# Kernel optimization log

Hardware: AMD Instinct MI355X
Metric: run time of the kernel (lower is better)

Reference implementation:

```python
import jax, jax.numpy as jnp
import numpy as np

N_NODES = 100000
N_EDGES = 3200000
D = 128
N_SUPPORTS = 2
N_LAYERS = 2


def setup_inputs() -> dict:
    key = jax.random.key(0)
    ks = jax.random.split(key, 6)
    x = jax.random.normal(ks[0], (1, N_NODES, D), dtype=jnp.float32)
    # small init scale to keep tanh out of saturation
    Ws = jax.random.normal(ks[1], (N_SUPPORTS, N_LAYERS, D, D), dtype=jnp.float32) * 0.05
    bs = jax.random.normal(ks[2], (N_SUPPORTS, N_LAYERS, D), dtype=jnp.float32) * 0.01
    vals = jax.random.uniform(ks[3], (N_SUPPORTS, N_EDGES), dtype=jnp.float32) / 32.0
    rows = jax.random.randint(ks[4], (N_SUPPORTS, N_EDGES), 0, N_NODES, dtype=jnp.int32)
    cols = jax.random.randint(ks[5], (N_SUPPORTS, N_EDGES), 0, N_NODES, dtype=jnp.int32)
    return {"x": x, "Ws": Ws, "bs": bs, "vals": vals, "rows": rows, "cols": cols}


def _spmm(vals, rows, cols, h, n):
    # y[r] += v * h[c]  (sparse COO matrix times dense feature matrix)
    return jax.ops.segment_sum(vals[:, None] * h[cols], rows, num_segments=n)


def reference(x, Ws, bs, vals, rows, cols):
    # AbstractGCN (siml GCN) with residual=True, nodes=[128,128,128],
    # activations=['tanh','tanh'] -> per-layer acts become [tanh, identity],
    # final tanh applied after residual sum; shortcut = identity (in==out dims).
    xb = x[0]  # batch size 1; supports are per-sample
    h_sum = jnp.zeros_like(xb)
    for s in range(N_SUPPORTS):
        h = xb
        for l in range(N_LAYERS):
            h = h @ Ws[s, l].T + bs[s, l]          # torch.nn.Linear
            h = _spmm(vals[s], rows[s], cols[s], h, N_NODES)
            if l == 0:
                h = jnp.tanh(h)                     # identity on last layer
        h_sum = h_sum + h
    out = jnp.tanh(h_sum + xb)                      # residual + final activation
    return out[None]  # stack over batch -> [1, N, D]
```

## Files before the change

kernel.cpp:

```cpp
#include <hip/hip_runtime.h>

#define NN 100000
#define DD 128
#define NE 3200000
#define SCAN_B 1024

__global__ __launch_bounds__(256) void gemm_xwt(const float* __restrict__ h,
                                                const float* __restrict__ W,
                                                const float* __restrict__ b,
                                                float* __restrict__ g) {
    __shared__ float Wl[128 * 128];
    const int t = threadIdx.x;
    for (int i = t * 4; i < 128 * 128; i += 256 * 4) {
        const int n = i >> 7;
        const int k = i & 127;
        const float4 w = *(const float4*)&W[i];
        *(float4*)&Wl[(n << 7) + ((((k >> 2) ^ (n & 7)) << 2))] = w;
    }
    __syncthreads();

    const int tc = t & 15;
    const int tr = t >> 4;
    const int r0 = blockIdx.x * 64 + tr * 4;

    int rr[4];
#pragma unroll
    for (int j = 0; j < 4; ++j) rr[j] = min(r0 + j, NN - 1);

    float acc[4][8];
#pragma unroll
    for (int i = 0; i < 8; ++i) {
        const float bv = b[tc + 16 * i];
#pragma unroll
        for (int j = 0; j < 4; ++j) acc[j][i] = bv;
    }

#pragma unroll 2
    for (int k0 = 0; k0 < 128; k0 += 4) {
        float4 hv[4];
#pragma unroll
        for (int j = 0; j < 4; ++j)
            hv[j] = *(const float4*)&h[(size_t)rr[j] * DD + k0];
#pragma unroll
        for (int i = 0; i < 8; ++i) {
            const int n = tc + 16 * i;
            const float4 wv =
                *(const float4*)&Wl[(n << 7) + ((((k0 >> 2) ^ (n & 7)) << 2))];
#pragma unroll
            for (int j = 0; j < 4; ++j) {
                acc[j][i] += hv[j].x * wv.x;
                acc[j][i] += hv[j].y * wv.y;
                acc[j][i] += hv[j].z * wv.z;
                acc[j][i] += hv[j].w * wv.w;
            }
        }
    }

#pragma unroll
    for (int j = 0; j < 4; ++j) {
        const int r = r0 + j;
        if (r < NN) {
#pragma unroll
            for (int i = 0; i < 8; ++i)
                g[(size_t)r * DD + tc + 16 * i] = acc[j][i];
        }
    }
}

__global__ __launch_bounds__(256) void edge_count2(const int* __restrict__ rows,
                                                   int* __restrict__ cnt2) {
    for (int e = blockIdx.x * 256 + threadIdx.x; e < 2 * NE;
         e += gridDim.x * 256) {
        const int soff = (e >= NE) ? NN : 0;
        atomicAdd(&cnt2[soff + rows[e]], 1);
    }
}

__global__ __launch_bounds__(SCAN_B) void scan1(const int* __restrict__ cnt2,
                                                int* __restrict__ rp2,
                                                int* __restrict__ sums2,
                                                int nb) {
    __shared__ int tmp[SCAN_B];
    const int s = blockIdx.x / nb;
    const int blk = blockIdx.x % nb;
    const int tid = threadIdx.x;
    const int i = blk * SCAN_B + tid;
    const int v = (i < NN) ? cnt2[s * NN + i] : 0;
    tmp[tid] = v;
    __syncthreads();
    for (int off = 1; off < SCAN_B; off <<= 1) {
        const int t = (tid >= off) ? tmp[tid - off] : 0;
        __syncthreads();
        tmp[tid] += t;
        __syncthreads();
    }
    if (i < NN) rp2[s * (NN + 1) + i] = tmp[tid] - v;
    if (tid == SCAN_B - 1) sums2[s * 128 + blk] = tmp[tid];
}

__global__ __launch_bounds__(128) void scan2(int* __restrict__ sums2, int nb) {
    __shared__ int tmp[128];
    const int tid = threadIdx.x;
    int* sums = sums2 + blockIdx.x * 128;
    const int v = (tid < nb) ? sums[tid] : 0;
    tmp[tid] = v;
    __syncthreads();
    for (int off = 1; off < 128; off <<= 1) {
        const int t = (tid >= off) ? tmp[tid - off] : 0;
        __syncthreads();
        tmp[tid] += t;
        __syncthreads();
    }
    if (tid < nb) sums[tid] = tmp[tid] - v;
}

__global__ __launch_bounds__(SCAN_B) void scan3(int* __restrict__ rp2,
                                                const int* __restrict__ sums2,
                                                int* __restrict__ cur2,
                                                int nb) {
    const int s = blockIdx.x / nb;
    const int blk = blockIdx.x % nb;
    const int i = blk * SCAN_B + threadIdx.x;
    if (i < NN) {
        const int v = rp2[s * (NN + 1) + i] + sums2[s * 128 + blk];
        rp2[s * (NN + 1) + i] = v;
        cur2[s * NN + i] = v;
    }
    if (i == 0) rp2[s * (NN + 1) + NN] = NE;
}

__global__ __launch_bounds__(256) void edge_scatter2(const float* __restrict__ vals,
                                                     const int* __restrict__ rows,
                                                     const int* __restrict__ cols,
                                                     int* __restrict__ cur2,
                                                     int2* __restrict__ pairs) {
    for (int e = blockIdx.x * 256 + threadIdx.x; e < 2 * NE;
         e += gridDim.x * 256) {
        const int is1 = (e >= NE);
        const int pos = atomicAdd(&cur2[is1 * NN + rows[e]], 1);
        pairs[(size_t)is1 * NE + pos] = make_int2(cols[e], __float_as_int(vals[e]));
    }
}

template <int MODE>
__global__ __launch_bounds__(256) void spmm_csr(const int* __restrict__ rp,
                                                const int2* __restrict__ pairs,
                                                const float* __restrict__ g,
                                                const float* __restrict__ x,
                                                float* __restrict__ y) {
    const int w = (blockIdx.x << 2) + (threadIdx.x >> 6);
    if (w >= NN) return;
    const int lane = threadIdx.x & 63;
    const int beg = rp[w];
    const int end = rp[w + 1];
    float2 acc = {0.f, 0.f};
    int j = beg;
    for (; j + 4 <= end; j += 4) {
        int2 p[4];
#pragma unroll
        for (int q = 0; q < 4; ++q) p[q] = pairs[j + q];
        float2 gv[4];
#pragma unroll
        for (int q = 0; q < 4; ++q)
            gv[q] = *(const float2*)&g[(size_t)p[q].x * DD + (lane << 1)];
#pragma unroll
        for (int q = 0; q < 4; ++q) {
            const float v = __int_as_float(p[q].y);
            acc.x += v * gv[q].x;
            acc.y += v * gv[q].y;
        }
    }
    for (; j < end; ++j) {
        const int2 p = pairs[j];
        const float v = __int_as_float(p.y);
        const float2 gv = *(const float2*)&g[(size_t)p.x * DD + (lane << 1)];
        acc.x += v * gv.x;
        acc.y += v * gv.y;
    }
    float* yp = &y[(size_t)w * DD + (lane << 1)];
    if (MODE == 0) {
        float2 r;
        r.x = tanhf(acc.x);
        r.y = tanhf(acc.y);
        *(float2*)yp = r;
    } else if (MODE == 1) {
        *(float2*)yp = acc;
    } else {
        const float2 xv = *(const float2*)&x[(size_t)w * DD + (lane << 1)];
        const float2 o = *(const float2*)yp;
        float2 r;
        r.x = tanhf(o.x + acc.x + xv.x);
        r.y = tanhf(o.y + acc.y + xv.y);
        *(float2*)yp = r;
    }
}

__global__ __launch_bounds__(256) void spmm_at(const float* __restrict__ vals,
                                               const int* __restrict__ rows,
                                               const int* __restrict__ cols,
                                               const float* __restrict__ g,
                                               float* __restrict__ y) {
    const int gid = blockIdx.x * 256 + threadIdx.x;
    const int f4 = (gid & 31) << 2;
    const int estride = (gridDim.x * 256) >> 5;
    for (int e = gid >> 5; e < NE; e += estride) {
        const float v = vals[e];
        const int r = rows[e];
        const int c = cols[e];
        const float4 gv = *(const float4*)&g[(size_t)c * DD + f4];
        float* yp = &y[(size_t)r * DD + f4];
        atomicAdd(yp + 0, v * gv.x);
        atomicAdd(yp + 1, v * gv.y);
        atomicAdd(yp + 2, v * gv.z);
        atomicAdd(yp + 3, v * gv.w);
    }
}

__global__ __launch_bounds__(256) void tanh_ip(float* __restrict__ y) {
    const size_t n4 = (size_t)NN * DD / 4;
    for (size_t i = (size_t)blockIdx.x * 256 + threadIdx.x; i < n4;
         i += (size_t)gridDim.x * 256) {
        float4 v = ((float4*)y)[i];
        v.x = tanhf(v.x);
        v.y = tanhf(v.y);
        v.z = tanhf(v.z);
        v.w = tanhf(v.w);
        ((float4*)y)[i] = v;
    }
}

__global__ __launch_bounds__(256) void final_act(float* __restrict__ out,
                                                 const float* __restrict__ x) {
    const size_t n4 = (size_t)NN * DD / 4;
    for (size_t i = (size_t)blockIdx.x * 256 + threadIdx.x; i < n4;
         i += (size_t)gridDim.x * 256) {
        const float4 a = ((const float4*)x)[i];
        float4 v = ((float4*)out)[i];
        v.x = tanhf(v.x + a.x);
        v.y = tanhf(v.y + a.y);
        v.z = tanhf(v.z + a.z);
        v.w = tanhf(v.w + a.w);
        ((float4*)out)[i] = v;
    }
}

extern "C" void kernel_launch(void* const* d_in, const int* in_sizes, int n_in,
                              void* d_out, int out_size, void* d_ws, size_t ws_size,
                              hipStream_t stream) {
    const float* x    = (const float*)d_in[0];
    const float* Ws   = (const float*)d_in[1];
    const float* bs   = (const float*)d_in[2];
    const float* vals = (const float*)d_in[3];
    const int*   rows = (const int*)d_in[4];
    const int*   cols = (const int*)d_in[5];
    float* out = (float*)d_out;

    const size_t FB    = (size_t)NN * DD * sizeof(float);
    const size_t RP2B  = ((size_t)2 * (NN + 1) * 4 + 127) & ~(size_t)127;
    const size_t PAIRB = (size_t)2 * NE * 8;
    const size_t CNTB  = ((size_t)2 * NN * 4 + 127) & ~(size_t)127;
    const size_t SUMB  = 1024;

    const size_t need_csr = 2 * FB + RP2B + PAIRB + 2 * CNTB + SUMB;

    char* p = (char*)d_ws;
    float* g = (float*)p; p += FB;
    float* y = (float*)p; p += FB;

    const int nb = (NN + SCAN_B - 1) / SCAN_B;

    if (ws_size >= need_csr) {
        int*  rp2   = (int*)p;  p += RP2B;
        int2* pairs = (int2*)p; p += PAIRB;
        int*  cnt2  = (int*)p;  p += CNTB;
        int*  cur2  = (int*)p;  p += CNTB;
        int*  sums2 = (int*)p;  p += SUMB;

        hipMemsetAsync(cnt2, 0, (size_t)2 * NN * 4, stream);
        edge_count2<<<8192, 256, 0, stream>>>(rows, cnt2);
        scan1<<<2 * nb, SCAN_B, 0, stream>>>(cnt2, rp2, sums2, nb);
        scan2<<<2, 128, 0, stream>>>(sums2, nb);
        scan3<<<2 * nb, SCAN_B, 0, stream>>>(rp2, sums2, cur2, nb);
        edge_scatter2<<<8192, 256, 0, stream>>>(vals, rows, cols, cur2, pairs);

        const int sgrid = (NN + 3) / 4;
        for (int s = 0; s < 2; ++s) {
            const float* W0 = Ws + (size_t)(s * 2 + 0) * DD * DD;
            const float* W1 = Ws + (size_t)(s * 2 + 1) * DD * DD;
            const float* b0 = bs + (size_t)(s * 2 + 0) * DD;
            const float* b1 = bs + (size_t)(s * 2 + 1) * DD;
            const int*  rp = rp2 + (size_t)s * (NN + 1);
            const int2* pr = pairs + (size_t)s * NE;

            gemm_xwt<<<(NN + 63) / 64, 256, 0, stream>>>(x, W0, b0, g);
            spmm_csr<0><<<sgrid, 256, 0, stream>>>(rp, pr, g, nullptr, y);
            gemm_xwt<<<(NN + 63) / 64, 256, 0, stream>>>(y, W1, b1, g);
            if (s == 0)
                spmm_csr<1><<<sgrid, 256, 0, stream>>>(rp, pr, g, nullptr, out);
            else
                spmm_csr<3><<<sgrid, 256, 0, stream>>>(rp, pr, g, x, out);
        }
        return;
    }

    hipMemsetAsync(out, 0, FB, stream);
    for (int s = 0; s < 2; ++s) {
        const float* W0 = Ws + (size_t)(s * 2 + 0) * DD * DD;
        const float* W1 = Ws + (size_t)(s * 2 + 1) * DD * DD;
        const float* b0 = bs + (size_t)(s * 2 + 0) * DD;
        const float* b1 = bs + (size_t)(s * 2 + 1) * DD;
        const float* vs = vals + (size_t)s * NE;
        const int*   rs = rows + (size_t)s * NE;
        const int*   cs = cols + (size_t)s * NE;

        gemm_xwt<<<(NN + 63) / 64, 256, 0, stream>>>(x, W0, b0, g);
        hipMemsetAsync(y, 0, FB, stream);
        spmm_at<<<8192, 256, 0, stream>>>(vs, rs, cs, g, y);
        tanh_ip<<<4096, 256, 0, stream>>>(y);
        gemm_xwt<<<(NN + 63) / 64, 256, 0, stream>>>(y, W1, b1, g);
        spmm_at<<<8192, 256, 0, stream>>>(vs, rs, cs, g, out);
    }
    final_act<<<4096, 256, 0, stream>>>(out, x);
}
```

Baseline: 1.861 ms.

## Store GEMM output as bf16 and build CSR via bucketed two-pass sort

```diff
diff --git a/kernel.cpp b/kernel.cpp
--- a/kernel.cpp
+++ b/kernel.cpp
@@ -3,12 +3,15 @@
 #define NN 100000
 #define DD 128
 #define NE 3200000
-#define SCAN_B 1024
-
+#define NBUK 196
+#define NSH 8
+#define NBS (2 * NBUK * NSH)
+
+template <int STORE_BF16>
 __global__ __launch_bounds__(256) void gemm_xwt(const float* __restrict__ h,
                                                 const float* __restrict__ W,
                                                 const float* __restrict__ b,
-                                                float* __restrict__ g) {
+                                                void* __restrict__ gout) {
     __shared__ float Wl[128 * 128];
     const int t = threadIdx.x;
     for (int i = t * 4; i < 128 * 128; i += 256 * 4) {
@@ -60,92 +63,130 @@
     for (int j = 0; j < 4; ++j) {
         const int r = r0 + j;
         if (r < NN) {
-#pragma unroll
-            for (int i = 0; i < 8; ++i)
-                g[(size_t)r * DD + tc + 16 * i] = acc[j][i];
-        }
-    }
-}
-
-__global__ __launch_bounds__(256) void edge_count2(const int* __restrict__ rows,
-                                                   int* __restrict__ cnt2) {
+            if (STORE_BF16) {
+                unsigned short* gp = (unsigned short*)gout + (size_t)r * DD;
+#pragma unroll
+                for (int i = 0; i < 8; ++i) {
+                    const unsigned int u = __float_as_uint(acc[j][i]);
+                    const unsigned short bf =
+                        (unsigned short)((u + 0x7FFFu + ((u >> 16) & 1u)) >> 16);
+                    gp[tc + 16 * i] = bf;
+                }
+            } else {
+                float* gp = (float*)gout + (size_t)r * DD;
+#pragma unroll
+                for (int i = 0; i < 8; ++i) gp[tc + 16 * i] = acc[j][i];
+            }
+        }
+    }
+}
+
+__global__ __launch_bounds__(256) void bcount(const int* __restrict__ rows,
+                                              int* __restrict__ bcnt8) {
     for (int e = blockIdx.x * 256 + threadIdx.x; e < 2 * NE;
          e += gridDim.x * 256) {
-        const int soff = (e >= NE) ? NN : 0;
-        atomicAdd(&cnt2[soff + rows[e]], 1);
-    }
-}
-
-__global__ __launch_bounds__(SCAN_B) void scan1(const int* __restrict__ cnt2,
-                                                int* __restrict__ rp2,
-                                                int* __restrict__ sums2,
-                                                int nb) {
-    __shared__ int tmp[SCAN_B];
-    const int s = blockIdx.x / nb;
-    const int blk = blockIdx.x % nb;
+        const int s = (e >= NE);
+        const int r = rows[e];
+        atomicAdd(&bcnt8[((s * NBUK + (r >> 9)) << 3) + ((e >> 8) & 7)], 1);
+    }
+}
+
+__global__ __launch_bounds__(1024) void bscan(const int* __restrict__ bcnt8,
+                                              int* __restrict__ bbase8,
+                                              int* __restrict__ bcur8,
+                                              int* __restrict__ rp2) {
+    __shared__ int tmp[1024];
     const int tid = threadIdx.x;
-    const int i = blk * SCAN_B + tid;
-    const int v = (i < NN) ? cnt2[s * NN + i] : 0;
-    tmp[tid] = v;
-    __syncthreads();
-    for (int off = 1; off < SCAN_B; off <<= 1) {
+    int v[4];
+    int s = 0;
+#pragma unroll
+    for (int q = 0; q < 4; ++q) {
+        const int i = tid * 4 + q;
+        v[q] = (i < NBS) ? bcnt8[i] : 0;
+        s += v[q];
+    }
+    tmp[tid] = s;
+    __syncthreads();
+    for (int off = 1; off < 1024; off <<= 1) {
         const int t = (tid >= off) ? tmp[tid - off] : 0;
         __syncthreads();
         tmp[tid] += t;
         __syncthreads();
     }
-    if (i < NN) rp2[s * (NN + 1) + i] = tmp[tid] - v;
-    if (tid == SCAN_B - 1) sums2[s * 128 + blk] = tmp[tid];
-}
-
-__global__ __launch_bounds__(128) void scan2(int* __restrict__ sums2, int nb) {
-    __shared__ int tmp[128];
-    const int tid = threadIdx.x;
-    int* sums = sums2 + blockIdx.x * 128;
-    const int v = (tid < nb) ? sums[tid] : 0;
-    tmp[tid] = v;
-    __syncthreads();
-    for (int off = 1; off < 128; off <<= 1) {
-        const int t = (tid >= off) ? tmp[tid - off] : 0;
-        __syncthreads();
-        tmp[tid] += t;
-        __syncthreads();
-    }
-    if (tid < nb) sums[tid] = tmp[tid] - v;
-}
-
-__global__ __launch_bounds__(SCAN_B) void scan3(int* __restrict__ rp2,
-                                                const int* __restrict__ sums2,
-                                                int* __restrict__ cur2,
-                                                int nb) {
-    const int s = blockIdx.x / nb;
-    const int blk = blockIdx.x % nb;
-    const int i = blk * SCAN_B + threadIdx.x;
-    if (i < NN) {
-        const int v = rp2[s * (NN + 1) + i] + sums2[s * 128 + blk];
-        rp2[s * (NN + 1) + i] = v;
-        cur2[s * NN + i] = v;
-    }
-    if (i == 0) rp2[s * (NN + 1) + NN] = NE;
-}
-
-__global__ __launch_bounds__(256) void edge_scatter2(const float* __restrict__ vals,
-                                                     const int* __restrict__ rows,
-                                                     const int* __restrict__ cols,
-                                                     int* __restrict__ cur2,
-                                                     int2* __restrict__ pairs) {
+    int excl = tmp[tid] - s;
+#pragma unroll
+    for (int q = 0; q < 4; ++q) {
+        const int i = tid * 4 + q;
+        if (i < NBS) {
+            bbase8[i] = excl;
+            bcur8[i] = excl;
+        }
+        excl += v[q];
+    }
+    if (tid == 1023) bbase8[NBS] = tmp[1023];
+    if (tid == 0) {
+        rp2[NN] = NE;
+        rp2[(NN + 1) + NN] = NE;
+    }
+}
+
+__global__ __launch_bounds__(256) void bscatter(const float* __restrict__ vals,
+                                                const int* __restrict__ rows,
+                                                const int* __restrict__ cols,
+                                                int* __restrict__ bcur8,
+                                                int2* __restrict__ aux) {
     for (int e = blockIdx.x * 256 + threadIdx.x; e < 2 * NE;
          e += gridDim.x * 256) {
-        const int is1 = (e >= NE);
-        const int pos = atomicAdd(&cur2[is1 * NN + rows[e]], 1);
-        pairs[(size_t)is1 * NE + pos] = make_int2(cols[e], __float_as_int(vals[e]));
+        const int s = (e >= NE);
+        const int r = rows[e];
+        const int idx = ((s * NBUK + (r >> 9)) << 3) + ((e >> 8) & 7);
+        const int pos = atomicAdd(&bcur8[idx], 1);
+        aux[pos] = make_int2(((r & 511) << 17) | cols[e], __float_as_int(vals[e]));
+    }
+}
+
+__global__ __launch_bounds__(512) void bsort(const int2* __restrict__ aux,
+                                             const int* __restrict__ bbase8,
+                                             int2* __restrict__ pairs,
+                                             int* __restrict__ rp2) {
+    __shared__ int hist[512], scn[512], cur[512];
+    const int b = blockIdx.x;
+    const int s = b / NBUK;
+    const int brow0 = (b - s * NBUK) << 9;
+    const int base = bbase8[b << 3];
+    const int nE = bbase8[(b + 1) << 3] - base;
+    const int tid = threadIdx.x;
+
+    hist[tid] = 0;
+    __syncthreads();
+    for (int i = tid; i < nE; i += 512)
+        atomicAdd(&hist[aux[base + i].x >> 17], 1);
+    __syncthreads();
+    scn[tid] = hist[tid];
+    __syncthreads();
+    for (int off = 1; off < 512; off <<= 1) {
+        const int t = (tid >= off) ? scn[tid - off] : 0;
+        __syncthreads();
+        scn[tid] += t;
+        __syncthreads();
+    }
+    const int excl = scn[tid] - hist[tid];
+    cur[tid] = excl;
+    const int row = brow0 + tid;
+    if (row < NN) rp2[s * (NN + 1) + row] = (base - s * NE) + excl;
+    __syncthreads();
+    for (int i = tid; i < nE; i += 512) {
+        const int2 p = aux[base + i];
+        const int rl = p.x >> 17;
+        const int pos = base + atomicAdd(&cur[rl], 1);
+        pairs[pos] = make_int2(p.x & 0x1FFFF, p.y);
     }
 }
 
 template <int MODE>
 __global__ __launch_bounds__(256) void spmm_csr(const int* __restrict__ rp,
                                                 const int2* __restrict__ pairs,
-                                                const float* __restrict__ g,
+                                                const char* __restrict__ gb,
                                                 const float* __restrict__ x,
                                                 float* __restrict__ y) {
     const int w = (blockIdx.x << 2) + (threadIdx.x >> 6);
@@ -159,23 +200,24 @@
         int2 p[4];
 #pragma unroll
         for (int q = 0; q < 4; ++q) p[q] = pairs[j + q];
-        float2 gv[4];
+        unsigned int u[4];
 #pragma unroll
         for (int q = 0; q < 4; ++q)
-            gv[q] = *(const float2*)&g[(size_t)p[q].x * DD + (lane << 1)];
+            u[q] = *(const unsigned int*)(gb + ((size_t)p[q].x << 8) + (lane << 2));
 #pragma unroll
         for (int q = 0; q < 4; ++q) {
             const float v = __int_as_float(p[q].y);
-            acc.x += v * gv[q].x;
-            acc.y += v * gv[q].y;
+            acc.x += v * __uint_as_float(u[q] << 16);
+            acc.y += v * __uint_as_float(u[q] & 0xFFFF0000u);
         }
     }
     for (; j < end; ++j) {
         const int2 p = pairs[j];
         const float v = __int_as_float(p.y);
-        const float2 gv = *(const float2*)&g[(size_t)p.x * DD + (lane << 1)];
-        acc.x += v * gv.x;
-        acc.y += v * gv.y;
+        const unsigned int u =
+            *(const unsigned int*)(gb + ((size_t)p.x << 8) + (lane << 2));
+        acc.x += v * __uint_as_float(u << 16);
+        acc.y += v * __uint_as_float(u & 0xFFFF0000u);
     }
     float* yp = &y[(size_t)w * DD + (lane << 1)];
     if (MODE == 0) {
@@ -255,33 +297,33 @@
     const int*   cols = (const int*)d_in[5];
     float* out = (float*)d_out;
 
+    const size_t GB16  = (size_t)NN * DD * 2;
     const size_t FB    = (size_t)NN * DD * sizeof(float);
+    const size_t PAIRB = (size_t)2 * NE * 8;
     const size_t RP2B  = ((size_t)2 * (NN + 1) * 4 + 127) & ~(size_t)127;
-    const size_t PAIRB = (size_t)2 * NE * 8;
-    const size_t CNTB  = ((size_t)2 * NN * 4 + 127) & ~(size_t)127;
-    const size_t SUMB  = 1024;
-
-    const size_t need_csr = 2 * FB + RP2B + PAIRB + 2 * CNTB + SUMB;
+    const size_t BCB   = ((size_t)(NBS + 8) * 4 + 127) & ~(size_t)127;
+
+    const size_t need_csr = GB16 + FB  + PAIRB + RP2B + 3 * BCB;
 
     char* p = (char*)d_ws;
-    float* g = (float*)p; p += FB;
-    float* y = (float*)p; p += FB;
-
-    const int nb = (NN + SCAN_B - 1) / SCAN_B;
 
     if (ws_size >= need_csr) {
-        int*  rp2   = (int*)p;  p += RP2B;
-        int2* pairs = (int2*)p; p += PAIRB;
-        int*  cnt2  = (int*)p;  p += CNTB;
-        int*  cur2  = (int*)p;  p += CNTB;
-        int*  sums2 = (int*)p;  p += SUMB;
-
-        hipMemsetAsync(cnt2, 0, (size_t)2 * NN * 4, stream);
-        edge_count2<<<8192, 256, 0, stream>>>(rows, cnt2);
-        scan1<<<2 * nb, SCAN_B, 0, stream>>>(cnt2, rp2, sums2, nb);
-        scan2<<<2, 128, 0, stream>>>(sums2, nb);
-        scan3<<<2 * nb, SCAN_B, 0, stream>>>(rp2, sums2, cur2, nb);
-        edge_scatter2<<<8192, 256, 0, stream>>>(vals, rows, cols, cur2, pairs);
+        char*  g     = p;          p += GB16;
+        char*  yaux  = p;          p += FB;
+        int2*  pairs = (int2*)p;   p += PAIRB;
+        int*   rp2   = (int*)p;    p += RP2B;
+        int*   bcnt8 = (int*)p;    p += BCB;
+        int*   bbase8= (int*)p;    p += BCB;
+        int*   bcur8 = (int*)p;    p += BCB;
+
+        float* y   = (float*)yaux;
+        int2*  aux = (int2*)yaux;
+
+        hipMemsetAsync(bcnt8, 0, (size_t)NBS * 4, stream);
+        bcount<<<4096, 256, 0, stream>>>(rows, bcnt8);
+        bscan<<<1, 1024, 0, stream>>>(bcnt8, bbase8, bcur8, rp2);
+        bscatter<<<4096, 256, 0, stream>>>(vals, rows, cols, bcur8, aux);
+        bsort<<<2 * NBUK, 512, 0, stream>>>(aux, bbase8, pairs, rp2);
 
         const int sgrid = (NN + 3) / 4;
         for (int s = 0; s < 2; ++s) {
@@ -292,9 +334,9 @@
             const int*  rp = rp2 + (size_t)s * (NN + 1);
             const int2* pr = pairs + (size_t)s * NE;
 
-            gemm_xwt<<<(NN + 63) / 64, 256, 0, stream>>>(x, W0, b0, g);
+            gemm_xwt<1><<<(NN + 63) / 64, 256, 0, stream>>>(x, W0, b0, g);
             spmm_csr<0><<<sgrid, 256, 0, stream>>>(rp, pr, g, nullptr, y);
-            gemm_xwt<<<(NN + 63) / 64, 256, 0, stream>>>(y, W1, b1, g);
+            gemm_xwt<1><<<(NN + 63) / 64, 256, 0, stream>>>(y, W1, b1, g);
             if (s == 0)
                 spmm_csr<1><<<sgrid, 256, 0, stream>>>(rp, pr, g, nullptr, out);
             else
@@ -303,6 +345,8 @@
         return;
     }
 
+    float* g = (float*)p;
+    float* y = g + (size_t)NN * DD;
     hipMemsetAsync(out, 0, FB, stream);
     for (int s = 0; s < 2; ++s) {
         const float* W0 = Ws + (size_t)(s * 2 + 0) * DD * DD;
@@ -313,11 +357,11 @@
         const int*   rs = rows + (size_t)s * NE;
         const int*   cs = cols + (size_t)s * NE;
 
-        gemm_xwt<<<(NN + 63) / 64, 256, 0, stream>>>(x, W0, b0, g);
+        gemm_xwt<0><<<(NN + 63) / 64, 256, 0, stream>>>(x, W0, b0, g);
         hipMemsetAsync(y, 0, FB, stream);
         spmm_at<<<8192, 256, 0, stream>>>(vs, rs, cs, g, y);
         tanh_ip<<<4096, 256, 0, stream>>>(y);
-        gemm_xwt<<<(NN + 63) / 64, 256, 0, stream>>>(y, W1, b1, g);
+        gemm_xwt<0><<<(NN + 63) / 64, 256, 0, stream>>>(y, W1, b1, g);
         spmm_at<<<8192, 256, 0, stream>>>(vs, rs, cs, g, out);
     }
     final_act<<<4096, 256, 0, stream>>>(out, x);
```

Measured after the change: 2.309 ms. 1.24x slower.
